# Kernel optimization log

Measured on AMD Instinct MI355X. Metric: run time of the kernel, lower is better.

Reference implementation:

```python
import jax, jax.numpy as jnp
from jax import lax
import numpy as np

V = 400_000   # total vertices (hits)
K = 64        # neighbours per vertex
NSEG = 4      # events (row-split segments)
SEG = V // NSEG


def setup_inputs() -> dict:
    key = jax.random.key(0)
    k1, k2 = jax.random.split(key)
    # neighbour indices constrained to each vertex's own row-split segment
    base = (jnp.arange(V, dtype=jnp.int32) // SEG) * SEG
    neighs = base[:, None] + jax.random.randint(k1, (V, K), 0, SEG, dtype=jnp.int32)
    neighs = neighs.at[:, 0].set(jnp.arange(V, dtype=jnp.int32))  # self as first neighbour (KNN convention)
    hier = jax.random.normal(k2, (V, 1), dtype=jnp.float32)
    row_splits = jnp.arange(NSEG + 1, dtype=jnp.int32) * SEG
    return {"neighs": neighs, "hier": hier, "row_splits": row_splits}


def _local_cluster(neighs, hier, row_splits):
    Vn = neighs.shape[0]
    vidx = jnp.arange(Vn, dtype=jnp.int32)
    # per-segment descending argsort of hier (== the raw_call per-row-split argsort loop)
    seg_id = (jnp.searchsorted(row_splits, vidx, side='right') - 1).astype(jnp.int32)
    order = jnp.lexsort((-hier[:, 0], seg_id)).astype(jnp.int32)  # primary: seg, secondary: hier desc
    order = lax.stop_gradient(order)

    def body(i, st):
        assigned, cluster_of, sel, n_sel = st
        v = order[i]
        is_new = jnp.logical_not(assigned[v])      # v not yet absorbed -> becomes a new centre
        cid = n_sel
        nb = neighs[v]                              # (K,)
        nb_ok = nb >= 0
        nbc = jnp.where(nb_ok, nb, v)               # safe index for padded (-1) neighbours
        take = is_new & nb_ok & jnp.logical_not(assigned[nbc])
        cluster_of = cluster_of.at[nbc].set(jnp.where(take, cid, cluster_of[nbc]))
        assigned = assigned.at[nbc].set(assigned[nbc] | take)
        # the centre itself always belongs to its own cluster
        cluster_of = cluster_of.at[v].set(jnp.where(is_new, cid, cluster_of[v]))
        assigned = assigned.at[v].set(True)
        sel = sel.at[cid].set(jnp.where(is_new, v, sel[cid]))
        n_sel = n_sel + is_new.astype(jnp.int32)
        return (assigned, cluster_of, sel, n_sel)

    init = (jnp.zeros(Vn, bool),
            jnp.zeros(Vn, jnp.int32),
            jnp.full((Vn,), -1, jnp.int32),   # sel padded with -1 (true length = n_sel)
            jnp.int32(0))
    assigned, cluster_of, sel, n_sel = lax.fori_loop(0, Vn, body, init)

    # new row splits: number of centres before each original boundary
    valid = sel >= 0
    is_center = (jnp.zeros(Vn, jnp.int32).at[jnp.where(valid, sel, 0)]
                 .add(valid.astype(jnp.int32))) > 0
    counts = jnp.cumsum(is_center.astype(jnp.int32))
    rs = jnp.concatenate([jnp.zeros(1, jnp.int32), counts[row_splits[1:] - 1]])
    return sel.reshape(-1, 1), rs, cluster_of.reshape(-1, 1)


_local_cluster_jit = jax.jit(_local_cluster)


def reference(neighs, hier, row_splits):
    # returns (sel [V,1] padded with -1, new row_splits [nseg+1], ggather [V,1])
    return _local_cluster_jit(neighs, hier, row_splits)
```

## Files before the change

kernel.cpp:

```cpp
#include <hip/hip_runtime.h>
#include <stdint.h>

typedef unsigned long long ull;

static __device__ __forceinline__ ull packkey(float f, int v) {
    uint32_t u = __float_as_uint(f);
    u = (u & 0x80000000u) ? ~u : (u | 0x80000000u);
    return ((ull)u << 32) | (ull)(~(uint32_t)v);
}
static __device__ __forceinline__ unsigned aloadu32(const unsigned* p) {
    return __hip_atomic_load(p, __ATOMIC_RELAXED, __HIP_MEMORY_SCOPE_AGENT);
}

__global__ void k_build4(const int* __restrict__ neighs, const float* __restrict__ hier,
                         unsigned* __restrict__ word, long E4, int K) {
    long t = (long)blockIdx.x * blockDim.x + threadIdx.x;
    if (t >= E4) return;
    long e = t * 4;
    int u = (int)(e / K);
    ull ku = packkey(hier[u], u);
    int4 w4 = *(const int4*)(neighs + e);
    int ws[4] = {w4.x, w4.y, w4.z, w4.w};
    #pragma unroll
    for (int j = 0; j < 4; j++) {
        int w = ws[j];
        if (w < 0) continue;
        if (ku > packkey(hier[w], w))
            atomicAdd(&word[w], 0x10000u);
    }
}
__global__ void k_build1(const int* __restrict__ neighs, const float* __restrict__ hier,
                         unsigned* __restrict__ word, long E, int K) {
    long e = (long)blockIdx.x * blockDim.x + threadIdx.x;
    if (e >= E) return;
    int w = neighs[e];
    if (w < 0) return;
    int u = (int)(e / K);
    if (packkey(hier[u], u) > packkey(hier[w], w))
        atomicAdd(&word[w], 0x10000u);
}

static __device__ __forceinline__ bool sweep_group(
    int gb, bool pend, int lane,
    const int* __restrict__ neighs, const float* __restrict__ hier,
    unsigned* __restrict__ word, ull* __restrict__ best, int K, bool& found)
{
    if (!__any(pend)) return pend;
    int v = gb + lane;
    unsigned wd = 0x7FFF0000u;
    if (pend) wd = aloadu32(&word[v]);
    bool absn = pend && ((wd & 0xFFFFu) != 0u);
    bool cenn = pend && (wd == 0u);
    bool dec = absn || cenn;
    ull mdec = __ballot(dec);
    if (!mdec) return pend;
    found = true;
    ull mcen = __ballot(cenn);

    while (mdec) {
        int ls[4];
        int nb = 0;
        while (nb < 4 && mdec) {
            int l = __ffsll((unsigned long long)mdec) - 1;
            mdec &= mdec - 1;
            ls[nb++] = l;
        }
        #pragma unroll
        for (int j = nb; j < 4; j++) ls[j] = -1;

        int vv[4]; ull kv[4]; unsigned dj[4]; bool cj[4];
        #pragma unroll
        for (int j = 0; j < 4; j++) {
            vv[j] = 0; kv[j] = 0; dj[j] = 0; cj[j] = false;
            if (ls[j] >= 0) {
                vv[j] = gb + ls[j];
                cj[j] = (mcen >> ls[j]) & 1ull;
                dj[j] = cj[j] ? 0xFFFF0001u : 0xFFFF0000u;
                kv[j] = packkey(hier[vv[j]], vv[j]);
            }
        }
        for (int k0 = 0; k0 < K; k0 += 64) {
            int k = k0 + lane;
            bool kok = k < K;
            #pragma unroll
            for (int j = 0; j < 4; j++) {
                if (ls[j] >= 0 && kok) {
                    int w = neighs[(size_t)vv[j] * (size_t)K + k];
                    if (w >= 0 && kv[j] > packkey(hier[w], w)) {
                        atomicAdd(&word[w], dj[j]);
                        if (cj[j]) atomicMax(&best[w], kv[j]);
                    }
                }
            }
        }
    }
    return pend && !dec;
}

__global__ __launch_bounds__(256, 8)
void k_propagate(const int* __restrict__ neighs, const float* __restrict__ hier,
                 unsigned* __restrict__ word, ull* __restrict__ best,
                 int V, int K, int nwaves) {
    const int gtid = blockIdx.x * blockDim.x + threadIdx.x;
    const int wv = gtid >> 6, lane = gtid & 63;
    const int G = (V + 63) >> 6;
    int gb0 = (wv < G) ? (wv << 6) : -1;
    int g1 = wv + nwaves;
    int gb1 = (g1 < G) ? (g1 << 6) : -1;
    bool p0 = gb0 >= 0 && gb0 + lane < V;
    bool p1 = gb1 >= 0 && gb1 + lane < V;

    long sweeps = 0;
    while (__any(p0 || p1)) {
        bool found = false;
        p0 = sweep_group(gb0, p0, lane, neighs, hier, word, best, K, found);
        p1 = sweep_group(gb1, p1, lane, neighs, hier, word, best, K, found);
        if (found) {
            sweeps = 0;
        } else {
            __builtin_amdgcn_s_sleep(2);
            if (++sweeps > 2000000L) break;
        }
    }
}

__global__ void k_compact(const float* __restrict__ hier,
                          const unsigned* __restrict__ word,
                          const int* __restrict__ row_splits,
                          ull* __restrict__ segKeys,
                          int* __restrict__ segIds,
                          int* __restrict__ counters,
                          int V, int NSEG) {
    int v = blockIdx.x * blockDim.x + threadIdx.x;
    int lane = threadIdx.x & 63;
    bool isc = (v < V) && ((word[v] & 0xFFFFu) == 0u);
    int s = 0;
    if (isc) { while (s + 1 < NSEG && v >= row_splits[s + 1]) s++; }
    if (!__any(isc)) return;
    for (int s0 = 0; s0 < NSEG; s0++) {
        ull ms = __ballot(isc && s == s0);
        if (!ms) continue;
        int leader = __ffsll((unsigned long long)ms) - 1;
        int n = __popcll(ms);
        unsigned base = 0;
        if (lane == leader) base = (unsigned)atomicAdd(&counters[s0], n);
        base = (unsigned)__shfl((int)base, leader);
        unsigned pre = (unsigned)__popcll(ms & ((1ull << lane) - 1ull));
        if (isc && s == s0) {
            int slot = row_splits[s0] + (int)(base + pre);
            segKeys[slot] = packkey(hier[v], v);
            segIds[slot] = v;
        }
    }
}

__global__ void k_rs(const int* __restrict__ counters,
                     int* __restrict__ rsBase,
                     int* __restrict__ rs_out,
                     int NSEG) {
    if (blockIdx.x == 0 && threadIdx.x == 0) {
        int acc = 0;
        rs_out[0] = 0;
        for (int s = 0; s < NSEG; s++) {
            rsBase[s] = acc;
            acc += counters[s];
            rs_out[s + 1] = acc;
        }
    }
}

#define RTILE 1024
__global__ void k_rank(const ull* __restrict__ segKeys,
                       const int* __restrict__ segIds,
                       const int* __restrict__ counters,
                       const int* __restrict__ rsBase,
                       const int* __restrict__ row_splits,
                       int* __restrict__ cidOf,
                       int* __restrict__ sel_out,
                       int V, int NSEG) {
    __shared__ ull tile[RTILE];
    int t = blockIdx.x * blockDim.x + threadIdx.x;
    int s = 0;
    if (t < V) { while (s + 1 < NSEG && t >= row_splits[s + 1]) s++; }
    int base = (t < V) ? row_splits[s] : 0;
    int j = (t < V) ? (t - base) : -1;
    int cnt = (t < V) ? counters[s] : 0;
    bool active = (t < V) && (j >= 0) && (j < cnt);
    ull mk = active ? segKeys[t] : 0ull;
    int r = 0;

    int B0 = blockIdx.x * blockDim.x;
    int B1 = min(B0 + (int)blockDim.x - 1, V - 1);
    int sf = 0; while (sf + 1 < NSEG && B0 >= row_splits[sf + 1]) sf++;
    int sl = 0; while (sl + 1 < NSEG && B1 >= row_splits[sl + 1]) sl++;

    for (int s0 = sf; s0 <= sl; s0++) {
        int b0 = row_splits[s0];
        int c0 = counters[s0];
        bool in = active && (s == s0);
        for (int tb = 0; tb < c0; tb += RTILE) {
            int n = min(RTILE, c0 - tb);
            __syncthreads();
            for (int i = threadIdx.x; i < n; i += blockDim.x)
                tile[i] = segKeys[b0 + tb + i];
            __syncthreads();
            if (in) {
                int rr = 0;
                #pragma unroll 8
                for (int i = 0; i < n; i++) rr += (tile[i] > mk) ? 1 : 0;
                r += rr;
            }
        }
    }
    if (active) {
        int cid = rsBase[s] + r;
        int v = segIds[t];
        cidOf[v] = cid;
        sel_out[cid] = v;
    }
}

__global__ void k_assign(const ull* __restrict__ best,
                         const int* __restrict__ cidOf,
                         int* __restrict__ clus_out,
                         int V) {
    int v = blockIdx.x * blockDim.x + threadIdx.x;
    if (v >= V) return;
    ull b = best[v];
    int c;
    if (b == 0ull) {
        c = cidOf[v];
    } else {
        uint32_t a = ~(uint32_t)(b & 0xFFFFFFFFull);
        c = cidOf[a];
    }
    clus_out[v] = c;
}

extern "C" void kernel_launch(void* const* d_in, const int* in_sizes, int n_in,
                              void* d_out, int out_size, void* d_ws, size_t ws_size,
                              hipStream_t stream) {
    const int*   neighs     = (const int*)d_in[0];
    const float* hier       = (const float*)d_in[1];
    const int*   row_splits = (const int*)d_in[2];

    const int V    = in_sizes[1];
    const int K    = in_sizes[0] / V;
    const int NSEG = in_sizes[2] - 1;
    const long E   = (long)V * (long)K;

    int* out      = (int*)d_out;
    int* sel_out  = out;
    int* rs_out   = out + V;
    int* clus_out = out + V + NSEG + 1;

    char* w = (char*)d_ws;
    ull*      best    = (ull*)(w);
    unsigned* word    = (unsigned*)(w + (size_t)8 * V);
    int*      cnts    = (int*)(w + (size_t)12 * V);
    int*      rsBase  = (int*)(w + (size_t)12 * V + 128);
    size_t segOff     = (size_t)12 * V + 256;
    ull*      segKeys = (ull*)(w + segOff);
    int*      segIds  = (int*)(w + segOff + (size_t)8 * V);
    int*      cidOf   = (int*)(w + segOff + (size_t)12 * V);

    const int B  = 256;
    const int gV = (V + B - 1) / B;

    (void)hipMemsetAsync(w, 0, segOff, stream);
    (void)hipMemsetAsync(sel_out, 0xFF, (size_t)4 * V, stream);

    if ((K & 3) == 0) {
        long E4 = E / 4;
        k_build4<<<(int)((E4 + B - 1) / B), B, 0, stream>>>(neighs, hier, word, E4, K);
    } else {
        k_build1<<<(int)((E + B - 1) / B), B, 0, stream>>>(neighs, hier, word, E, K);
    }

    const int PB = 2048;
    const int NW = PB * B / 64;
    k_propagate<<<PB, B, 0, stream>>>(neighs, hier, word, best, V, K, NW);

    k_compact<<<gV, B, 0, stream>>>(hier, word, row_splits, segKeys, segIds, cnts, V, NSEG);
    k_rs<<<1, 64, 0, stream>>>(cnts, rsBase, rs_out, NSEG);
    k_rank<<<gV, B, 0, stream>>>(segKeys, segIds, cnts, rsBase, row_splits,
                                 cidOf, sel_out, V, NSEG);
    k_assign<<<gV, B, 0, stream>>>(best, cidOf, clus_out, V);
}
```

Before: 1.284 ms.

## Assign one vertex group per wave in propagate and fold k_rs into k_rank

The propagate kernel now launches one wave per 64-vertex group instead of each wave polling two groups. The grid is sized to the group count (about 1563 blocks rather than 2048). The separate single-thread k_rs launch is removed: k_rank now computes each segment's base offset from the counters itself, and block 0 writes the new row splits. This saves a kernel launch and removes the serialization of two groups sharing one wave. The risk is that all waves must be resident at once for the spin-wait propagation to make progress, since a wave can wait on another wave that has not been scheduled.

Result: no change. 1.284 ms (median of 2 runs) (-0.0%).

```diff
diff --git a/kernel.cpp b/kernel.cpp
--- a/kernel.cpp
+++ b/kernel.cpp
@@ -40,86 +40,70 @@
         atomicAdd(&word[w], 0x10000u);
 }
 
-static __device__ __forceinline__ bool sweep_group(
-    int gb, bool pend, int lane,
-    const int* __restrict__ neighs, const float* __restrict__ hier,
-    unsigned* __restrict__ word, ull* __restrict__ best, int K, bool& found)
-{
-    if (!__any(pend)) return pend;
-    int v = gb + lane;
-    unsigned wd = 0x7FFF0000u;
-    if (pend) wd = aloadu32(&word[v]);
-    bool absn = pend && ((wd & 0xFFFFu) != 0u);
-    bool cenn = pend && (wd == 0u);
-    bool dec = absn || cenn;
-    ull mdec = __ballot(dec);
-    if (!mdec) return pend;
-    found = true;
-    ull mcen = __ballot(cenn);
-
-    while (mdec) {
-        int ls[4];
-        int nb = 0;
-        while (nb < 4 && mdec) {
-            int l = __ffsll((unsigned long long)mdec) - 1;
-            mdec &= mdec - 1;
-            ls[nb++] = l;
-        }
-        #pragma unroll
-        for (int j = nb; j < 4; j++) ls[j] = -1;
-
-        int vv[4]; ull kv[4]; unsigned dj[4]; bool cj[4];
-        #pragma unroll
-        for (int j = 0; j < 4; j++) {
-            vv[j] = 0; kv[j] = 0; dj[j] = 0; cj[j] = false;
-            if (ls[j] >= 0) {
-                vv[j] = gb + ls[j];
-                cj[j] = (mcen >> ls[j]) & 1ull;
-                dj[j] = cj[j] ? 0xFFFF0001u : 0xFFFF0000u;
-                kv[j] = packkey(hier[vv[j]], vv[j]);
-            }
-        }
-        for (int k0 = 0; k0 < K; k0 += 64) {
-            int k = k0 + lane;
-            bool kok = k < K;
-            #pragma unroll
-            for (int j = 0; j < 4; j++) {
-                if (ls[j] >= 0 && kok) {
-                    int w = neighs[(size_t)vv[j] * (size_t)K + k];
-                    if (w >= 0 && kv[j] > packkey(hier[w], w)) {
-                        atomicAdd(&word[w], dj[j]);
-                        if (cj[j]) atomicMax(&best[w], kv[j]);
-                    }
-                }
-            }
-        }
-    }
-    return pend && !dec;
-}
-
 __global__ __launch_bounds__(256, 8)
 void k_propagate(const int* __restrict__ neighs, const float* __restrict__ hier,
                  unsigned* __restrict__ word, ull* __restrict__ best,
-                 int V, int K, int nwaves) {
+                 int V, int K) {
     const int gtid = blockIdx.x * blockDim.x + threadIdx.x;
     const int wv = gtid >> 6, lane = gtid & 63;
-    const int G = (V + 63) >> 6;
-    int gb0 = (wv < G) ? (wv << 6) : -1;
-    int g1 = wv + nwaves;
-    int gb1 = (g1 < G) ? (g1 << 6) : -1;
-    bool p0 = gb0 >= 0 && gb0 + lane < V;
-    bool p1 = gb1 >= 0 && gb1 + lane < V;
+    const int gb = wv << 6;
+    if (gb >= V) return;
+    int v = gb + lane;
+    bool pend = v < V;
 
     long sweeps = 0;
-    while (__any(p0 || p1)) {
-        bool found = false;
-        p0 = sweep_group(gb0, p0, lane, neighs, hier, word, best, K, found);
-        p1 = sweep_group(gb1, p1, lane, neighs, hier, word, best, K, found);
-        if (found) {
-            sweeps = 0;
-        } else {
+    while (__any(pend)) {
+        unsigned wd = 0x7FFF0000u;
+        if (pend) wd = aloadu32(&word[v]);
+        bool absn = pend && ((wd & 0xFFFFu) != 0u);
+        bool cenn = pend && (wd == 0u);
+        bool dec = absn || cenn;
+        ull mdec = __ballot(dec);
+        if (!mdec) {
             __builtin_amdgcn_s_sleep(2);
             if (++sweeps > 2000000L) break;
+            continue;
+        }
+        sweeps = 0;
+        ull mcen = __ballot(cenn);
+        if (dec) pend = false;
+
+        while (mdec) {
+            int ls[4];
+            int nb = 0;
+            while (nb < 4 && mdec) {
+                int l = __ffsll((unsigned long long)mdec) - 1;
+                mdec &= mdec - 1;
+                ls[nb++] = l;
+            }
+            #pragma unroll
+            for (int j = nb; j < 4; j++) ls[j] = -1;
+
+            int vv[4]; ull kv[4]; unsigned dj[4]; bool cj[4];
+            #pragma unroll
+            for (int j = 0; j < 4; j++) {
+                vv[j] = 0; kv[j] = 0; dj[j] = 0; cj[j] = false;
+                if (ls[j] >= 0) {
+                    vv[j] = gb + ls[j];
+                    cj[j] = (mcen >> ls[j]) & 1ull;
+                    dj[j] = cj[j] ? 0xFFFF0001u : 0xFFFF0000u;
+                    kv[j] = packkey(hier[vv[j]], vv[j]);
+                }
+            }
+            for (int k0 = 0; k0 < K; k0 += 64) {
+                int k = k0 + lane;
+                bool kok = k < K;
+                #pragma unroll
+                for (int j = 0; j < 4; j++) {
+                    if (ls[j] >= 0 && kok) {
+                        int w = neighs[(size_t)vv[j] * (size_t)K + k];
+                        if (w >= 0 && kv[j] > packkey(hier[w], w)) {
+                            atomicAdd(&word[w], dj[j]);
+                            if (cj[j]) atomicMax(&best[w], kv[j]);
+                        }
+                    }
+                }
+            }
         }
     }
 }
@@ -154,34 +138,28 @@
     }
 }
 
-__global__ void k_rs(const int* __restrict__ counters,
-                     int* __restrict__ rsBase,
-                     int* __restrict__ rs_out,
-                     int NSEG) {
-    if (blockIdx.x == 0 && threadIdx.x == 0) {
-        int acc = 0;
-        rs_out[0] = 0;
-        for (int s = 0; s < NSEG; s++) {
-            rsBase[s] = acc;
-            acc += counters[s];
-            rs_out[s + 1] = acc;
-        }
-    }
-}
-
 #define RTILE 1024
 __global__ void k_rank(const ull* __restrict__ segKeys,
                        const int* __restrict__ segIds,
                        const int* __restrict__ counters,
-                       const int* __restrict__ rsBase,
                        const int* __restrict__ row_splits,
                        int* __restrict__ cidOf,
                        int* __restrict__ sel_out,
+                       int* __restrict__ rs_out,
                        int V, int NSEG) {
     __shared__ ull tile[RTILE];
+    int rsb = 0;
     int t = blockIdx.x * blockDim.x + threadIdx.x;
     int s = 0;
     if (t < V) { while (s + 1 < NSEG && t >= row_splits[s + 1]) s++; }
+    for (int i = 0; i < s; i++) rsb += counters[i];
+
+    if (blockIdx.x == 0 && threadIdx.x == 0) {
+        int acc = 0;
+        rs_out[0] = 0;
+        for (int i = 0; i < NSEG; i++) { acc += counters[i]; rs_out[i + 1] = acc; }
+    }
+
     int base = (t < V) ? row_splits[s] : 0;
     int j = (t < V) ? (t - base) : -1;
     int cnt = (t < V) ? counters[s] : 0;
@@ -213,7 +191,7 @@
         }
     }
     if (active) {
-        int cid = rsBase[s] + r;
+        int cid = rsb + r;
         int v = segIds[t];
         cidOf[v] = cid;
         sel_out[cid] = v;
@@ -258,8 +236,7 @@
     ull*      best    = (ull*)(w);
     unsigned* word    = (unsigned*)(w + (size_t)8 * V);
     int*      cnts    = (int*)(w + (size_t)12 * V);
-    int*      rsBase  = (int*)(w + (size_t)12 * V + 128);
-    size_t segOff     = (size_t)12 * V + 256;
+    size_t segOff     = (size_t)12 * V + 128;
     ull*      segKeys = (ull*)(w + segOff);
     int*      segIds  = (int*)(w + segOff + (size_t)8 * V);
     int*      cidOf   = (int*)(w + segOff + (size_t)12 * V);
@@ -277,13 +254,12 @@
         k_build1<<<(int)((E + B - 1) / B), B, 0, stream>>>(neighs, hier, word, E, K);
     }
 
-    const int PB = 2048;
-    const int NW = PB * B / 64;
-    k_propagate<<<PB, B, 0, stream>>>(neighs, hier, word, best, V, K, NW);
+    const int G  = (V + 63) >> 6;
+    const int PB = (G + 3) / 4;
+    k_propagate<<<PB, B, 0, stream>>>(neighs, hier, word, best, V, K);
 
     k_compact<<<gV, B, 0, stream>>>(hier, word, row_splits, segKeys, segIds, cnts, V, NSEG);
-    k_rs<<<1, 64, 0, stream>>>(cnts, rsBase, rs_out, NSEG);
-    k_rank<<<gV, B, 0, stream>>>(segKeys, segIds, cnts, rsBase, row_splits,
-                                 cidOf, sel_out, V, NSEG);
+    k_rank<<<gV, B, 0, stream>>>(segKeys, segIds, cnts, row_splits,
+                                 cidOf, sel_out, rs_out, V, NSEG);
     k_assign<<<gV, B, 0, stream>>>(best, cidOf, clus_out, V);
 }
```
